# Performance work log

Hardware: AMD Instinct MI355X
Metric: run time of the kernel (lower is better)

Reference implementation:

```python
import jax, jax.numpy as jnp
import numpy as np

N, D, E, R, G, M = 8192, 1024, 64, 64, 8, 8

def setup_inputs() -> dict:
    key = jax.random.key(0)
    k_h, k_wg, k_wl, k_w1, k_w2 = jax.random.split(key, 5)
    return {
        'h': jax.random.normal(k_h, (N, D), jnp.float32),
        'Wg': jax.random.normal(k_wg, (D, G), jnp.float32) * 0.02,  # nn.Linear weight (transposed)
        'bg': jnp.zeros((G,), jnp.float32),
        'Wloc': jax.random.normal(k_wl, (G, D, M), jnp.float32) * 0.02,
        'W1': jax.random.normal(k_w1, (E, D, R), jnp.float32) * 0.02,
        'W2': jax.random.normal(k_w2, (E, R, D), jnp.float32) * 0.02,
        'k': 2,
    }

def reference(h, Wg, bg, Wloc, W1, W2, k):
    n, d = h.shape
    g, _, m = Wloc.shape
    e = W1.shape[0]
    router_temp = 1.0
    # stage 1: group routing (top-1)
    g_scores = h @ Wg + bg                                   # (N, G)
    group_idx = jnp.argmax(g_scores, axis=-1)                # (N,)
    # stage 2: within-group scores; compute all groups (cheap: N*G*M) then select
    all_local = jnp.einsum('nd,gdm->ngm', h, Wloc)           # (N, G, M)
    local_scores = jnp.take_along_axis(all_local, group_idx[:, None, None], axis=1)[:, 0]  # (N, M)
    topv, topm = jax.lax.top_k(local_scores, k)              # (N, k)
    gate = jax.nn.softmax(topv / max(router_temp, 1e-6), axis=-1)
    expert_ids = group_idx[:, None] * m + topm               # (N, k) global expert ids
    # scatter gates into dense (N, E); topm entries are distinct per token
    gate_full = jnp.zeros((n, e), h.dtype).at[jnp.arange(n)[:, None], expert_ids].set(gate)
    # low-rank expert compute: relu(h @ W1) @ W2, weighted-combined
    tmp = jax.nn.relu(jnp.einsum('nd,edr->ner', h, W1))      # (N, E, R)
    out = jnp.einsum('ner,erd->nd', gate_full[:, :, None] * tmp, W2)  # (N, D)
    return out, expert_ids, gate, group_idx
```

## Files before the change

kernel.cpp:

```cpp
#include <hip/hip_runtime.h>
#include <hip/hip_bf16.h>
#include <cstdint>
#include <cstddef>

#define NTOK 8192
#define DIM  1024
#define NEXP 64
#define RANK 64
#define NGRP 8
#define NLOC 8

typedef __attribute__((ext_vector_type(8))) short bf16x8;
typedef __attribute__((ext_vector_type(4))) float f32x4;

static __device__ inline unsigned int pack_bf16x2(float a, float b) {
    __hip_bfloat16 ha = __float2bfloat16(a);
    __hip_bfloat16 hb = __float2bfloat16(b);
    return (unsigned int)(*(unsigned short*)&ha) |
           ((unsigned int)(*(unsigned short*)&hb) << 16);
}

__global__ __launch_bounds__(256, 8) void score_route(
    const float* __restrict__ h, const float* __restrict__ Wg,
    const float* __restrict__ bg, const float* __restrict__ Wloc,
    unsigned short* __restrict__ hb, float* __restrict__ out_gidx,
    float* __restrict__ out_eid, float* __restrict__ out_gate,
    int* __restrict__ ws_eids, float* __restrict__ ws_gates,
    int* __restrict__ counts_e)
{
    __shared__ float hLds[4][1024];

    const int tid  = threadIdx.x;
    const int wave = tid >> 6;
    const int lane = tid & 63;
    const int tok  = blockIdx.x * 4 + wave;

    const float* hrow = h + (size_t)tok * DIM;
    unsigned short* hbrow = hb + (size_t)tok * DIM;

    float4 hv[4];
#pragma unroll
    for (int i = 0; i < 4; ++i)
        hv[i] = *(const float4*)(hrow + lane * 4 + i * 256);
#pragma unroll
    for (int i = 0; i < 4; ++i) {
        const int k0 = lane * 4 + i * 256;
        *(float4*)&hLds[wave][k0] = hv[i];
        uint2 pk;
        pk.x = pack_bf16x2(hv[i].x, hv[i].y);
        pk.y = pack_bf16x2(hv[i].z, hv[i].w);
        *(uint2*)(hbrow + k0) = pk;
    }

    const int row_l = lane >> 1;
    const int half  = lane & 1;

    float ga[4] = {};
#pragma unroll 8
    for (int i = 0; i < 32; ++i) {
        const float a  = hLds[wave][i * 32 + row_l];
        const float4 b = *(const float4*)(Wg + i * 256 + lane * 4);
        ga[0] += a * b.x; ga[1] += a * b.y; ga[2] += a * b.z; ga[3] += a * b.w;
    }
#pragma unroll
    for (int d = 2; d < 64; d <<= 1) {
#pragma unroll
        for (int m = 0; m < 4; ++m) ga[m] += __shfl_xor(ga[m], d, 64);
    }
    float gb[4];
#pragma unroll
    for (int m = 0; m < 4; ++m) gb[m] = __shfl_xor(ga[m], 1, 64);

    float sc[8];
#pragma unroll
    for (int m = 0; m < 4; ++m) {
        sc[m]     = (half ? gb[m] : ga[m]) + bg[m];
        sc[m + 4] = (half ? ga[m] : gb[m]) + bg[m + 4];
    }
    int gi = 0; float best = sc[0];
#pragma unroll
    for (int g = 1; g < NGRP; ++g) {
        if (sc[g] > best) { best = sc[g]; gi = g; }
    }

    const float* wl = Wloc + (size_t)gi * (DIM * NLOC);
    float la[4] = {};
#pragma unroll 8
    for (int i = 0; i < 32; ++i) {
        const float a  = hLds[wave][i * 32 + row_l];
        const float4 b = *(const float4*)(wl + i * 256 + lane * 4);
        la[0] += a * b.x; la[1] += a * b.y; la[2] += a * b.z; la[3] += a * b.w;
    }
#pragma unroll
    for (int d = 2; d < 64; d <<= 1) {
#pragma unroll
        for (int m = 0; m < 4; ++m) la[m] += __shfl_xor(la[m], d, 64);
    }
    float lb[4];
#pragma unroll
    for (int m = 0; m < 4; ++m) lb[m] = __shfl_xor(la[m], 1, 64);

    float ls[8];
#pragma unroll
    for (int m = 0; m < 4; ++m) {
        ls[m]     = half ? lb[m] : la[m];
        ls[m + 4] = half ? la[m] : lb[m];
    }

    int m1 = 0; float v1 = ls[0];
#pragma unroll
    for (int m = 1; m < NLOC; ++m) { if (ls[m] > v1) { v1 = ls[m]; m1 = m; } }
    int m2 = (m1 == 0) ? 1 : 0; float v2 = ls[m2];
#pragma unroll
    for (int m = 0; m < NLOC; ++m) {
        if (m != m1 && m != ((m1 == 0) ? 1 : 0) && ls[m] > v2) { v2 = ls[m]; m2 = m; }
    }

    if (lane == 0) {
        const float e2v = expf(v2 - v1);
        const float inv = 1.f / (1.f + e2v);
        const float g0 = inv, g1 = e2v * inv;
        const int ea = gi * NLOC + m1, eb = gi * NLOC + m2;

        out_gidx[tok] = (float)gi;
        out_eid[tok * 2 + 0] = (float)ea;
        out_eid[tok * 2 + 1] = (float)eb;
        out_gate[tok * 2 + 0] = g0;
        out_gate[tok * 2 + 1] = g1;
        ws_eids[tok * 2 + 0] = ea;
        ws_eids[tok * 2 + 1] = eb;
        ws_gates[tok * 2 + 0] = g0;
        ws_gates[tok * 2 + 1] = g1;
        atomicAdd(&counts_e[ea], 1);
        atomicAdd(&counts_e[eb], 1);
    }
}

__global__ __launch_bounds__(256) void scatter_e(
    const int* __restrict__ ws_eids, const float* __restrict__ ws_gates,
    const int* __restrict__ counts_e, int* __restrict__ cursor,
    int* __restrict__ token_list, float* __restrict__ slot_gate)
{
    __shared__ int offS[64];
    const int tid = threadIdx.x;
    if (tid < 64) {
        const int c = counts_e[tid];
        int s = c;
#pragma unroll
        for (int d = 1; d < 64; d <<= 1) {
            int v = __shfl_up(s, d, 64);
            if (tid >= d) s += v;
        }
        offS[tid] = s - c;
    }
    __syncthreads();
    const int t = blockIdx.x * 256 + tid;
    if (t >= NTOK) return;
#pragma unroll
    for (int j = 0; j < 2; ++j) {
        const int eid = ws_eids[t * 2 + j];
        const int pos = offS[eid] + atomicAdd(&cursor[eid], 1);
        token_list[pos] = t * 2 + j;
        slot_gate[pos] = ws_gates[t * 2 + j];
    }
}

__global__ __launch_bounds__(256) void prep_w(
    const float* __restrict__ W1, const float* __restrict__ W2,
    unsigned short* __restrict__ W1t, unsigned short* __restrict__ W2t)
{
    __shared__ float Ls[64][65];
    const int e = blockIdx.x;
    const int y = blockIdx.y;
    if (y < 16) {
        const int kb = y;
        const float* src = W1 + (size_t)e * DIM * RANK + (size_t)kb * 64 * RANK;
#pragma unroll
        for (int it = 0; it < 4; ++it) {
            const int kk = (threadIdx.x >> 4) + it * 16;
            const int rr = (threadIdx.x & 15) * 4;
            *(float4*)&Ls[kk][rr] = *(const float4*)(src + (size_t)kk * RANK + rr);
        }
        __syncthreads();
#pragma unroll
        for (int it = 0; it < 2; ++it) {
            const int idx = threadIdx.x + it * 256;
            const int r = idx >> 3, k8 = (idx & 7) * 8;
            uint4 v;
            v.x = pack_bf16x2(Ls[k8 + 0][r], Ls[k8 + 1][r]);
            v.y = pack_bf16x2(Ls[k8 + 2][r], Ls[k8 + 3][r]);
            v.z = pack_bf16x2(Ls[k8 + 4][r], Ls[k8 + 5][r]);
            v.w = pack_bf16x2(Ls[k8 + 6][r], Ls[k8 + 7][r]);
            *(uint4*)(W1t + (size_t)e * RANK * DIM + (size_t)r * DIM + kb * 64 + k8) = v;
        }
    } else {
        const int db = y - 16;
        const float* src = W2 + (size_t)e * RANK * DIM + db * 64;
#pragma unroll
        for (int it = 0; it < 4; ++it) {
            const int rr = (threadIdx.x >> 4) + it * 16;
            const int dd = (threadIdx.x & 15) * 4;
            *(float4*)&Ls[rr][dd] = *(const float4*)(src + (size_t)rr * DIM + dd);
        }
        __syncthreads();
#pragma unroll
        for (int it = 0; it < 2; ++it) {
            const int idx = threadIdx.x + it * 256;
            const int d = idx >> 3, r8 = (idx & 7) * 8;
            uint4 v;
            v.x = pack_bf16x2(Ls[r8 + 0][d], Ls[r8 + 1][d]);
            v.y = pack_bf16x2(Ls[r8 + 2][d], Ls[r8 + 3][d]);
            v.z = pack_bf16x2(Ls[r8 + 4][d], Ls[r8 + 5][d]);
            v.w = pack_bf16x2(Ls[r8 + 6][d], Ls[r8 + 7][d]);
            *(uint4*)(W2t + (size_t)e * DIM * RANK + (size_t)(db * 64 + d) * RANK + r8) = v;
        }
    }
}

__global__ __launch_bounds__(256, 2) void e1_mfma(
    const unsigned short* __restrict__ hb, const unsigned short* __restrict__ W1t,
    const int* __restrict__ counts_e, const int* __restrict__ token_list,
    const float* __restrict__ slot_gate, unsigned short* __restrict__ P)
{
    __shared__ unsigned short Hs[64 * 72];
    __shared__ unsigned short Ws[64 * 72];
    __shared__ int   tokS[64];
    __shared__ float gateS[64];
    __shared__ int   offS[65];

    const int e   = blockIdx.x;
    const int tid = threadIdx.x;
    if (tid < 64) {
        const int c = counts_e[tid];
        int s = c;
#pragma unroll
        for (int d = 1; d < 64; d <<= 1) {
            int v = __shfl_up(s, d, 64);
            if (tid >= d) s += v;
        }
        offS[tid] = s - c;
        if (tid == 63) offS[64] = s;
    }
    __syncthreads();
    const int n0 = offS[e];
    const int ne = offS[e + 1] - n0;

    const unsigned short* W1te = W1t + (size_t)e * RANK * DIM;
    const int wave = tid >> 6;
    const int lane = tid & 63;
    const int tx   = lane & 15;
    const int quad = lane >> 4;

    for (int tile = blockIdx.y; tile * 64 < ne; tile += 8) {
        const int row0 = tile * 64;
        __syncthreads();
        if (tid < 64) {
            const int gr = row0 + tid;
            tokS[tid]  = (gr < ne) ? token_list[n0 + gr] : -1;
            gateS[tid] = (gr < ne) ? slot_gate[n0 + gr] : 0.f;
        }
        f32x4 acc[4] = {};
        for (int kc = 0; kc < DIM; kc += 64) {
            __syncthreads();
#pragma unroll
            for (int it = 0; it < 2; ++it) {
                const int idx = tid + it * 256;
                const int s = idx >> 3, k8 = (idx & 7) * 8;
                const int ent = tokS[s];
                uint4 v = make_uint4(0, 0, 0, 0);
                if (ent >= 0)
                    v = *(const uint4*)(hb + (size_t)(ent >> 1) * DIM + kc + k8);
                *(uint4*)(Hs + s * 72 + k8) = v;
            }
#pragma unroll
            for (int it = 0; it < 2; ++it) {
                const int idx = tid + it * 256;
                const int r = idx >> 3, k8 = (idx & 7) * 8;
                *(uint4*)(Ws + r * 72 + k8) =
                    *(const uint4*)(W1te + (size_t)r * DIM + kc + k8);
            }
            __syncthreads();
#pragma unroll
            for (int ks = 0; ks < 2; ++ks) {
                const bf16x8 a = *(const bf16x8*)(Hs + (wave * 16 + tx) * 72 + ks * 32 + quad * 8);
#pragma unroll
                for (int j = 0; j < 4; ++j) {
                    const bf16x8 b = *(const bf16x8*)(Ws + (j * 16 + tx) * 72 + ks * 32 + quad * 8);
                    acc[j] = __builtin_amdgcn_mfma_f32_16x16x32_bf16(a, b, acc[j], 0, 0, 0);
                }
            }
        }
#pragma unroll
        for (int j = 0; j < 4; ++j) {
#pragma unroll
            for (int i = 0; i < 4; ++i) {
                const int sl = wave * 16 + quad * 4 + i;
                const int gr = row0 + sl;
                if (gr < ne) {
                    const float v = fmaxf(acc[j][i], 0.f) * gateS[sl];
                    __hip_bfloat16 hv = __float2bfloat16(v);
                    P[(size_t)(n0 + gr) * RANK + j * 16 + tx] = *(unsigned short*)&hv;
                }
            }
        }
    }
}

__global__ __launch_bounds__(256, 2) void e2_mfma(
    const unsigned short* __restrict__ P, const unsigned short* __restrict__ W2t,
    const int* __restrict__ counts_e, const int* __restrict__ token_list,
    float* __restrict__ out, float* __restrict__ contrib)
{
    __shared__ unsigned short Ps[64 * 72];
    __shared__ unsigned short W2s[64 * 72];
    __shared__ int tokS[64];
    __shared__ int offS[65];

    const int e = blockIdx.x;
    const int colbase = blockIdx.y * 64;
    const int tid = threadIdx.x;
    if (tid < 64) {
        const int c = counts_e[tid];
        int s = c;
#pragma unroll
        for (int d = 1; d < 64; d <<= 1) {
            int v = __shfl_up(s, d, 64);
            if (tid >= d) s += v;
        }
        offS[tid] = s - c;
        if (tid == 63) offS[64] = s;
    }
    __syncthreads();
    const int n0 = offS[e];
    const int ne = offS[e + 1] - n0;

    const unsigned short* W2te = W2t + (size_t)e * DIM * RANK;
    const int wave = tid >> 6;
    const int lane = tid & 63;
    const int tx   = lane & 15;
    const int quad = lane >> 4;

#pragma unroll
    for (int it = 0; it < 2; ++it) {
        const int idx = tid + it * 256;
        const int d = idx >> 3, r8 = (idx & 7) * 8;
        *(uint4*)(W2s + d * 72 + r8) =
            *(const uint4*)(W2te + (size_t)(colbase + d) * RANK + r8);
    }

    for (int tile = blockIdx.z; tile * 64 < ne; tile += 4) {
        const int row0 = tile * 64;
        __syncthreads();
        if (tid < 64) {
            const int gr = row0 + tid;
            tokS[tid] = (gr < ne) ? token_list[n0 + gr] : -1;
        }
#pragma unroll
        for (int it = 0; it < 2; ++it) {
            const int idx = tid + it * 256;
            const int s = idx >> 3, r8 = (idx & 7) * 8;
            const int gr = row0 + s;
            uint4 v = make_uint4(0, 0, 0, 0);
            if (gr < ne) v = *(const uint4*)(P + (size_t)(n0 + gr) * RANK + r8);
            *(uint4*)(Ps + s * 72 + r8) = v;
        }
        __syncthreads();
        f32x4 acc[4] = {};
#pragma unroll
        for (int ks = 0; ks < 2; ++ks) {
            const bf16x8 a = *(const bf16x8*)(Ps + (wave * 16 + tx) * 72 + ks * 32 + quad * 8);
#pragma unroll
            for (int j = 0; j < 4; ++j) {
                const bf16x8 b = *(const bf16x8*)(W2s + (j * 16 + tx) * 72 + ks * 32 + quad * 8);
                acc[j] = __builtin_amdgcn_mfma_f32_16x16x32_bf16(a, b, acc[j], 0, 0, 0);
            }
        }
#pragma unroll
        for (int i = 0; i < 4; ++i) {
            const int sl = wave * 16 + quad * 4 + i;
            const int ent = tokS[sl];
            if (ent >= 0) {
                float* base = (ent & 1) ? contrib : out;
                float* op = base + (size_t)(ent >> 1) * DIM + colbase;
#pragma unroll
                for (int j = 0; j < 4; ++j)
                    op[j * 16 + tx] = acc[j][i];
            }
        }
    }
}

__global__ __launch_bounds__(256) void combine_kernel(
    const float* __restrict__ contrib, float* __restrict__ out)
{
    const size_t i = (size_t)blockIdx.x * 256 + threadIdx.x;
    float4 a = ((const float4*)out)[i];
    const float4 b = ((const float4*)contrib)[i];
    a.x += b.x; a.y += b.y; a.z += b.z; a.w += b.w;
    ((float4*)out)[i] = a;
}

extern "C" void kernel_launch(void* const* d_in, const int* in_sizes, int n_in,
                              void* d_out, int out_size, void* d_ws, size_t ws_size,
                              hipStream_t stream)
{
    const float* h    = (const float*)d_in[0];
    const float* Wg   = (const float*)d_in[1];
    const float* bg   = (const float*)d_in[2];
    const float* Wloc = (const float*)d_in[3];
    const float* W1   = (const float*)d_in[4];
    const float* W2   = (const float*)d_in[5];

    float* out_f    = (float*)d_out;
    float* out_main = out_f;
    float* out_eid  = out_f + (size_t)NTOK * DIM;
    float* out_gate = out_eid + (size_t)NTOK * 2;
    float* out_gidx = out_gate + (size_t)NTOK * 2;

    int* ws_i        = (int*)d_ws;
    int* counts_e    = ws_i;
    int* cursor_e    = ws_i + 192;
    int* ws_eids     = ws_i + 16896;
    int* token_list  = ws_i + 33280;
    float* ws_f      = (float*)(ws_i + 49664);
    float* ws_gates  = ws_f;
    float* slot_gate = ws_f + 16384;
    unsigned short* P_h = (unsigned short*)(ws_f + 2 * 16384 + 65536);
    unsigned short* W1t = P_h + (size_t)16384 * RANK;
    unsigned short* W2t = W1t + (size_t)NEXP * RANK * DIM;
    float* contrib      = (float*)(W2t + (size_t)NEXP * DIM * RANK);
    unsigned short* hb = (unsigned short*)contrib;

    hipMemsetAsync(ws_i, 0, 256 * sizeof(int), stream);

    prep_w<<<dim3(NEXP, 32), 256, 0, stream>>>(W1, W2, W1t, W2t);
    score_route<<<NTOK / 4, 256, 0, stream>>>(h, Wg, bg, Wloc, hb,
        out_gidx, out_eid, out_gate, ws_eids, ws_gates, counts_e);
    scatter_e<<<NTOK / 256, 256, 0, stream>>>(ws_eids, ws_gates, counts_e,
        cursor_e, token_list, slot_gate);
    e1_mfma<<<dim3(NEXP, 8), 256, 0, stream>>>(hb, W1t, counts_e, token_list,
        slot_gate, P_h);
    e2_mfma<<<dim3(NEXP, 16, 4), 256, 0, stream>>>(P_h, W2t, counts_e, token_list,
        out_main, contrib);
    combine_kernel<<<(NTOK * DIM / 4) / 256, 256, 0, stream>>>(contrib, out_main);
}
```

Before: 289.9 us.

## Compute all routing scores as tiled GEMM then route in separate kernel

```diff
diff --git a/kernel.cpp b/kernel.cpp
--- a/kernel.cpp
+++ b/kernel.cpp
@@ -20,92 +20,150 @@
            ((unsigned int)(*(unsigned short*)&hb) << 16);
 }
 
-__global__ __launch_bounds__(256, 8) void score_route(
+__global__ __launch_bounds__(256, 2) void score_all(
     const float* __restrict__ h, const float* __restrict__ Wg,
-    const float* __restrict__ bg, const float* __restrict__ Wloc,
-    unsigned short* __restrict__ hb, float* __restrict__ out_gidx,
-    float* __restrict__ out_eid, float* __restrict__ out_gate,
-    int* __restrict__ ws_eids, float* __restrict__ ws_gates,
-    int* __restrict__ counts_e)
-{
-    __shared__ float hLds[4][1024];
-
+    const float* __restrict__ Wloc, unsigned short* __restrict__ hb,
+    float* __restrict__ Sp)
+{
+    __shared__ float Hs[64][65];
+    __shared__ float Ws[64][44];
+
+    const int tile = blockIdx.x;
+    const int slab = blockIdx.y;
+    const int z    = blockIdx.z;
     const int tid  = threadIdx.x;
     const int wave = tid >> 6;
     const int lane = tid & 63;
-    const int tok  = blockIdx.x * 4 + wave;
-
-    const float* hrow = h + (size_t)tok * DIM;
-    unsigned short* hbrow = hb + (size_t)tok * DIM;
-
-    float4 hv[4];
-#pragma unroll
-    for (int i = 0; i < 4; ++i)
-        hv[i] = *(const float4*)(hrow + lane * 4 + i * 256);
-#pragma unroll
-    for (int i = 0; i < 4; ++i) {
-        const int k0 = lane * 4 + i * 256;
-        *(float4*)&hLds[wave][k0] = hv[i];
-        uint2 pk;
-        pk.x = pack_bf16x2(hv[i].x, hv[i].y);
-        pk.y = pack_bf16x2(hv[i].z, hv[i].w);
-        *(uint2*)(hbrow + k0) = pk;
-    }
-
-    const int row_l = lane >> 1;
-    const int half  = lane & 1;
-
-    float ga[4] = {};
-#pragma unroll 8
-    for (int i = 0; i < 32; ++i) {
-        const float a  = hLds[wave][i * 32 + row_l];
-        const float4 b = *(const float4*)(Wg + i * 256 + lane * 4);
-        ga[0] += a * b.x; ga[1] += a * b.y; ga[2] += a * b.z; ga[3] += a * b.w;
-    }
-#pragma unroll
-    for (int d = 2; d < 64; d <<= 1) {
-#pragma unroll
-        for (int m = 0; m < 4; ++m) ga[m] += __shfl_xor(ga[m], d, 64);
-    }
-    float gb[4];
-#pragma unroll
-    for (int m = 0; m < 4; ++m) gb[m] = __shfl_xor(ga[m], 1, 64);
-
-    float sc[8];
-#pragma unroll
-    for (int m = 0; m < 4; ++m) {
-        sc[m]     = (half ? gb[m] : ga[m]) + bg[m];
-        sc[m + 4] = (half ? ga[m] : gb[m]) + bg[m + 4];
-    }
-    int gi = 0; float best = sc[0];
+    const int t0   = tile * 64;
+    const int kz   = z * 512;
+    const int ncol = slab ? 32 : 40;
+
+    float acc[10] = {};
+
+    for (int chunk = 0; chunk < 8; ++chunk) {
+        const int kb = kz + chunk * 64;
+        __syncthreads();
+        {
+            const int r = tid >> 2, seg = (tid & 3) * 16;
+            const float* src = h + (size_t)(t0 + r) * DIM + kb + seg;
+            const float4 v0 = *(const float4*)(src);
+            const float4 v1 = *(const float4*)(src + 4);
+            const float4 v2 = *(const float4*)(src + 8);
+            const float4 v3 = *(const float4*)(src + 12);
+            float* dst = &Hs[r][seg];
+            dst[0]  = v0.x; dst[1]  = v0.y; dst[2]  = v0.z; dst[3]  = v0.w;
+            dst[4]  = v1.x; dst[5]  = v1.y; dst[6]  = v1.z; dst[7]  = v1.w;
+            dst[8]  = v2.x; dst[9]  = v2.y; dst[10] = v2.z; dst[11] = v2.w;
+            dst[12] = v3.x; dst[13] = v3.y; dst[14] = v3.z; dst[15] = v3.w;
+            if (slab == 0) {
+                unsigned short* hrow = hb + (size_t)(t0 + r) * DIM + kb + seg;
+                uint2 p0, p1, p2, p3;
+                p0.x = pack_bf16x2(v0.x, v0.y); p0.y = pack_bf16x2(v0.z, v0.w);
+                p1.x = pack_bf16x2(v1.x, v1.y); p1.y = pack_bf16x2(v1.z, v1.w);
+                p2.x = pack_bf16x2(v2.x, v2.y); p2.y = pack_bf16x2(v2.z, v2.w);
+                p3.x = pack_bf16x2(v3.x, v3.y); p3.y = pack_bf16x2(v3.z, v3.w);
+                *(uint2*)(hrow)      = p0;
+                *(uint2*)(hrow + 4)  = p1;
+                *(uint2*)(hrow + 8)  = p2;
+                *(uint2*)(hrow + 12) = p3;
+            }
+        }
+        {
+            const int krow = tid & 63;
+            const int c4b  = tid >> 6;
+#pragma unroll
+            for (int p = 0; p < 3; ++p) {
+                const int c4 = c4b + p * 4;
+                if (c4 * 4 < ncol) {
+                    const int o = c4 >> 1, m4 = (c4 & 1) * 4;
+                    const float* wsrc;
+                    if (slab == 0) {
+                        wsrc = (o == 0)
+                            ? (Wg + (size_t)(kb + krow) * NGRP + m4)
+                            : (Wloc + (size_t)(o - 1) * (DIM * NLOC)
+                                    + (size_t)(kb + krow) * NLOC + m4);
+                    } else {
+                        wsrc = Wloc + (size_t)(4 + o) * (DIM * NLOC)
+                                    + (size_t)(kb + krow) * NLOC + m4;
+                    }
+                    *(float4*)&Ws[krow][c4 * 4] = *(const float4*)wsrc;
+                }
+            }
+        }
+        __syncthreads();
+        if (slab == 0) {
+            const int c0 = wave * 10;
+#pragma unroll 4
+            for (int k = 0; k < 64; ++k) {
+                const float a = Hs[lane][k];
+                const float2 b0 = *(const float2*)&Ws[k][c0];
+                const float2 b1 = *(const float2*)&Ws[k][c0 + 2];
+                const float2 b2 = *(const float2*)&Ws[k][c0 + 4];
+                const float2 b3 = *(const float2*)&Ws[k][c0 + 6];
+                const float2 b4 = *(const float2*)&Ws[k][c0 + 8];
+                acc[0] += a * b0.x; acc[1] += a * b0.y;
+                acc[2] += a * b1.x; acc[3] += a * b1.y;
+                acc[4] += a * b2.x; acc[5] += a * b2.y;
+                acc[6] += a * b3.x; acc[7] += a * b3.y;
+                acc[8] += a * b4.x; acc[9] += a * b4.y;
+            }
+        } else {
+            const int c0 = wave * 8;
+#pragma unroll 4
+            for (int k = 0; k < 64; ++k) {
+                const float a = Hs[lane][k];
+                const float4 b0 = *(const float4*)&Ws[k][c0];
+                const float4 b1 = *(const float4*)&Ws[k][c0 + 4];
+                acc[0] += a * b0.x; acc[1] += a * b0.y;
+                acc[2] += a * b0.z; acc[3] += a * b0.w;
+                acc[4] += a * b1.x; acc[5] += a * b1.y;
+                acc[6] += a * b1.z; acc[7] += a * b1.w;
+            }
+        }
+    }
+    const int gcol = (slab ? 40 + wave * 8 : wave * 10);
+    float* dstS = Sp + (size_t)z * (NTOK * 72) + (size_t)(t0 + lane) * 72 + gcol;
+    if (slab == 0) {
+#pragma unroll
+        for (int c = 0; c < 10; ++c) dstS[c] = acc[c];
+    } else {
+#pragma unroll
+        for (int c = 0; c < 8; ++c) dstS[c] = acc[c];
+    }
+}
+
+__global__ __launch_bounds__(256) void route_all(
+    const float* __restrict__ Sp, const float* __restrict__ bg,
+    float* __restrict__ out_gidx, float* __restrict__ out_eid,
+    float* __restrict__ out_gate, int* __restrict__ ws_eids,
+    float* __restrict__ ws_gates, int* __restrict__ counts_e)
+{
+    __shared__ int hist[NEXP];
+    if (threadIdx.x < NEXP) hist[threadIdx.x] = 0;
+    __syncthreads();
+
+    const int t = blockIdx.x * 256 + threadIdx.x;
+    const float* p0 = Sp + (size_t)t * 72;
+    const float* p1 = Sp + (size_t)NTOK * 72 + (size_t)t * 72;
+    float s[72];
+#pragma unroll
+    for (int i = 0; i < 18; ++i) {
+        const float4 a = *(const float4*)(p0 + i * 4);
+        const float4 b = *(const float4*)(p1 + i * 4);
+        s[i * 4 + 0] = a.x + b.x; s[i * 4 + 1] = a.y + b.y;
+        s[i * 4 + 2] = a.z + b.z; s[i * 4 + 3] = a.w + b.w;
+    }
+
+    int gi = 0; float best = s[0] + bg[0];
 #pragma unroll
     for (int g = 1; g < NGRP; ++g) {
-        if (sc[g] > best) { best = sc[g]; gi = g; }
-    }
-
-    const float* wl = Wloc + (size_t)gi * (DIM * NLOC);
-    float la[4] = {};
-#pragma unroll 8
-    for (int i = 0; i < 32; ++i) {
-        const float a  = hLds[wave][i * 32 + row_l];
-        const float4 b = *(const float4*)(wl + i * 256 + lane * 4);
-        la[0] += a * b.x; la[1] += a * b.y; la[2] += a * b.z; la[3] += a * b.w;
-    }
-#pragma unroll
-    for (int d = 2; d < 64; d <<= 1) {
-#pragma unroll
-        for (int m = 0; m < 4; ++m) la[m] += __shfl_xor(la[m], d, 64);
-    }
-    float lb[4];
-#pragma unroll
-    for (int m = 0; m < 4; ++m) lb[m] = __shfl_xor(la[m], 1, 64);
-
-    float ls[8];
-#pragma unroll
-    for (int m = 0; m < 4; ++m) {
-        ls[m]     = half ? lb[m] : la[m];
-        ls[m + 4] = half ? la[m] : lb[m];
-    }
+        const float v = s[g] + bg[g];
+        if (v > best) { best = v; gi = g; }
+    }
+
+    float ls[NLOC];
+#pragma unroll
+    for (int m = 0; m < NLOC; ++m) ls[m] = s[8 + gi * NLOC + m];
 
     int m1 = 0; float v1 = ls[0];
 #pragma unroll
@@ -115,25 +173,25 @@
     for (int m = 0; m < NLOC; ++m) {
         if (m != m1 && m != ((m1 == 0) ? 1 : 0) && ls[m] > v2) { v2 = ls[m]; m2 = m; }
     }
-
-    if (lane == 0) {
-        const float e2v = expf(v2 - v1);
-        const float inv = 1.f / (1.f + e2v);
-        const float g0 = inv, g1 = e2v * inv;
-        const int ea = gi * NLOC + m1, eb = gi * NLOC + m2;
-
-        out_gidx[tok] = (float)gi;
-        out_eid[tok * 2 + 0] = (float)ea;
-        out_eid[tok * 2 + 1] = (float)eb;
-        out_gate[tok * 2 + 0] = g0;
-        out_gate[tok * 2 + 1] = g1;
-        ws_eids[tok * 2 + 0] = ea;
-        ws_eids[tok * 2 + 1] = eb;
-        ws_gates[tok * 2 + 0] = g0;
-        ws_gates[tok * 2 + 1] = g1;
-        atomicAdd(&counts_e[ea], 1);
-        atomicAdd(&counts_e[eb], 1);
-    }
+    const float e2v = expf(v2 - v1);
+    const float inv = 1.f / (1.f + e2v);
+    const float g0 = inv, g1 = e2v * inv;
+    const int ea = gi * NLOC + m1, eb = gi * NLOC + m2;
+
+    out_gidx[t] = (float)gi;
+    out_eid[t * 2 + 0] = (float)ea;
+    out_eid[t * 2 + 1] = (float)eb;
+    out_gate[t * 2 + 0] = g0;
+    out_gate[t * 2 + 1] = g1;
+    ws_eids[t * 2 + 0] = ea;
+    ws_eids[t * 2 + 1] = eb;
+    ws_gates[t * 2 + 0] = g0;
+    ws_gates[t * 2 + 1] = g1;
+    atomicAdd(&hist[ea], 1);
+    atomicAdd(&hist[eb], 1);
+
+    __syncthreads();
+    if (threadIdx.x < NEXP) atomicAdd(&counts_e[threadIdx.x], hist[threadIdx.x]);
 }
 
 __global__ __launch_bounds__(256) void scatter_e(
@@ -425,7 +483,8 @@
     float* ws_f      = (float*)(ws_i + 49664);
     float* ws_gates  = ws_f;
     float* slot_gate = ws_f + 16384;
-    unsigned short* P_h = (unsigned short*)(ws_f + 2 * 16384 + 65536);
+    float* Sp        = ws_f + 2 * 16384;
+    unsigned short* P_h = (unsigned short*)(Sp + (size_t)2 * NTOK * 72);
     unsigned short* W1t = P_h + (size_t)16384 * RANK;
     unsigned short* W2t = W1t + (size_t)NEXP * RANK * DIM;
     float* contrib      = (float*)(W2t + (size_t)NEXP * DIM * RANK);
@@ -434,8 +493,9 @@
     hipMemsetAsync(ws_i, 0, 256 * sizeof(int), stream);
 
     prep_w<<<dim3(NEXP, 32), 256, 0, stream>>>(W1, W2, W1t, W2t);
-    score_route<<<NTOK / 4, 256, 0, stream>>>(h, Wg, bg, Wloc, hb,
-        out_gidx, out_eid, out_gate, ws_eids, ws_gates, counts_e);
+    score_all<<<dim3(128, 2, 2), 256, 0, stream>>>(h, Wg, Wloc, hb, Sp);
+    route_all<<<NTOK / 256, 256, 0, stream>>>(Sp, bg, out_gidx, out_eid,
+        out_gate, ws_eids, ws_gates, counts_e);
     scatter_e<<<NTOK / 256, 256, 0, stream>>>(ws_eids, ws_gates, counts_e,
         cursor_e, token_list, slot_gate);
     e1_mfma<<<dim3(NEXP, 8), 256, 0, stream>>>(hb, W1t, counts_e, token_list,
```

New measurement: 259.6 us. 1.12x faster.
